# Optimization experiments

Measured on AMD Instinct MI355X. Metric: run time of the kernel, lower is better.

Reference implementation:

```python
import jax, jax.numpy as jnp
import numpy as np

N_ATOMS = 50000
N_EDGES = 640000
D = 128
N_RBF = 20
N_INTER = 3

act = jax.nn.softplus


def setup_inputs() -> dict:
    key = jax.random.key(0)
    ks = jax.random.split(key, 16)
    s = 1.0 / np.sqrt(D)
    inp = {
        "x": jax.random.normal(ks[0], (N_ATOMS, D), jnp.float32),
        "g_ij": jax.random.uniform(ks[1], (N_EDGES, N_RBF), jnp.float32),
        "idx_i": jax.random.randint(ks[2], (N_EDGES,), 0, N_ATOMS),
        "idx_j": jax.random.randint(ks[3], (N_EDGES,), 0, N_ATOMS),
        "n_atoms": N_ATOMS,
        "u": jnp.ones((D,), jnp.float32),
        "Wf": jax.random.normal(ks[4], (D, D), jnp.float32) * s,
        "bf": jnp.zeros((D,), jnp.float32),
        # linear_g weight init to zero in original; use small random so grads flow
        "Wg": jax.random.normal(ks[5], (D, N_RBF), jnp.float32) * 0.01,
        "bg": jnp.zeros((D,), jnp.float32),
        "Wj": jax.random.normal(ks[6], (D, D), jnp.float32) * s,
        "bj": jnp.zeros((D,), jnp.float32),
        "Wi": jax.random.normal(ks[7], (D, D), jnp.float32) * s,
        "bi": jnp.zeros((D,), jnp.float32),
        "res_w1": jax.random.normal(ks[8], (N_INTER, D, D), jnp.float32) * s,
        "res_b1": jnp.zeros((N_INTER, D), jnp.float32),
        "res_w2": jax.random.normal(ks[9], (N_INTER, D, D), jnp.float32) * s,
        "res_b2": jnp.zeros((N_INTER, D), jnp.float32),
    }
    return inp


def reference(x, g_ij, idx_i, idx_j, n_atoms, u, Wf, bf, Wg, bg, Wj, bj, Wi, bi,
              res_w1, res_b1, res_w2, res_b2):
    x_j = x[idx_j]                                    # [E, D] gather
    xp = u * x                                        # [N, D]
    # sequential_j: act -> linear_j -> act, gated by linear_g(g_ij)
    vp = act(act(x_j) @ Wj.T + bj) * (g_ij @ Wg.T + bg)   # [E, D]
    vm = act(act(x) @ Wi.T + bi)                      # [N, D]
    v = jax.ops.segment_sum(vp, idx_i, num_segments=n_atoms) + vm
    for l in range(res_w1.shape[0]):
        h = act(v) @ res_w1[l].T + res_b1[l]
        h = act(h) @ res_w2[l].T + res_b2[l]
        v = h + v
    v = act(v)
    return xp + v @ Wf.T + bf
```

## Files before the change

### kernel.cpp

```cpp
#include <hip/hip_runtime.h>
#include <hip/hip_fp16.h>

#define DD 128

typedef __attribute__((ext_vector_type(8))) short short8;
typedef __attribute__((ext_vector_type(8))) unsigned short ushort8;
typedef __attribute__((ext_vector_type(4))) float floatx4;
typedef unsigned int uint32;

__device__ __forceinline__ float sp(float x) {
    return fmaxf(x, 0.0f) + __logf(1.0f + __expf(-fabsf(x)));
}

__device__ __forceinline__ unsigned short f2bf(float f) {
    union { float f; uint32 u; } c; c.f = f;
    const uint32 u = c.u;
    return (unsigned short)((u + 0x7fffu + ((u >> 16) & 1u)) >> 16);
}

__device__ __forceinline__ unsigned short f2h(float f) {
    __half h = __float2half(f);
    return __builtin_bit_cast(unsigned short, h);
}

__global__ __launch_bounds__(256)
void convert_w(const float* __restrict__ Wj, const float* __restrict__ Wi,
               const float* __restrict__ rw1, const float* __restrict__ rw2,
               const float* __restrict__ Wf, unsigned short* __restrict__ out,
               const float* __restrict__ g, unsigned short* __restrict__ gh,
               int gchunks)
{
    if ((int)blockIdx.x >= 72) {
        const int gid = ((int)blockIdx.x - 72) * 256 + threadIdx.x;
        if (gid < gchunks) {
            const float4 f0 = reinterpret_cast<const float4*>(g)[2 * gid];
            const float4 f1 = reinterpret_cast<const float4*>(g)[2 * gid + 1];
            ushort8 o;
            o[0] = f2h(f0.x); o[1] = f2h(f0.y); o[2] = f2h(f0.z); o[3] = f2h(f0.w);
            o[4] = f2h(f1.x); o[5] = f2h(f1.y); o[6] = f2h(f1.z); o[7] = f2h(f1.w);
            reinterpret_cast<ushort8*>(gh)[gid] = o;
        }
        return;
    }
    const int gid = blockIdx.x * 256 + threadIdx.x;
    const int mat = gid >> 11;
    const int f8  = gid & 2047;
    const float* src;
    if      (mat == 0) src = Wj;
    else if (mat == 1) src = Wi;
    else if (mat <= 4) src = rw1 + (size_t)(mat - 2) * 16384;
    else if (mat <= 7) src = rw2 + (size_t)(mat - 5) * 16384;
    else               src = Wf;
    const int row = f8 >> 4;
    const int ch  = f8 & 15;
    const float4 a = reinterpret_cast<const float4*>(src)[2 * f8];
    const float4 b = reinterpret_cast<const float4*>(src)[2 * f8 + 1];
    ushort8 u8;
    u8[0] = f2bf(a.x); u8[1] = f2bf(a.y); u8[2] = f2bf(a.z); u8[3] = f2bf(a.w);
    u8[4] = f2bf(b.x); u8[5] = f2bf(b.y); u8[6] = f2bf(b.z); u8[7] = f2bf(b.w);
    *reinterpret_cast<ushort8*>(out + (size_t)mat * 16384 + row * 128 +
                                ((ch ^ (row & 15)) << 3)) = u8;
}

__device__ __forceinline__ void stage_wb(const unsigned short* __restrict__ Wb,
                                         unsigned short* wl, int t)
{
    #pragma unroll
    for (int i = 0; i < 8; ++i) {
        const int c = t + i * 256;
        *reinterpret_cast<ushort8*>(wl + c * 8) =
            *reinterpret_cast<const ushort8*>(Wb + c * 8);
    }
}

__device__ __forceinline__ void load_afrag_act(const float* __restrict__ X,
                                               int m, int q, int n, short8 af[4])
{
    const int mm = m < n ? m : n - 1;
    const float* row = X + (size_t)mm * DD + q * 8;
    #pragma unroll
    for (int kk = 0; kk < 4; ++kk) {
        const float4 a = *reinterpret_cast<const float4*>(row + kk * 32);
        const float4 b = *reinterpret_cast<const float4*>(row + kk * 32 + 4);
        ushort8 u;
        u[0] = f2bf(sp(a.x)); u[1] = f2bf(sp(a.y)); u[2] = f2bf(sp(a.z)); u[3] = f2bf(sp(a.w));
        u[4] = f2bf(sp(b.x)); u[5] = f2bf(sp(b.y)); u[6] = f2bf(sp(b.z)); u[7] = f2bf(sp(b.w));
        af[kk] = __builtin_bit_cast(short8, u);
    }
}

__device__ __forceinline__ void mfma_gemm(const unsigned short* wl,
                                          const short8 af[4],
                                          int cl, int q, floatx4 acc[8])
{
    #pragma unroll
    for (int nt = 0; nt < 8; ++nt) {
        const int nrow = nt * 16 + cl;
        #pragma unroll
        for (int kk = 0; kk < 4; ++kk) {
            const int chs = (kk * 4 + q) ^ cl;
            const short8 bfr = *reinterpret_cast<const short8*>(wl + nrow * 128 + (chs << 3));
            acc[nt] = __builtin_amdgcn_mfma_f32_16x16x32_bf16(af[kk], bfr, acc[nt], 0, 0, 0);
        }
    }
}

__global__ __launch_bounds__(256, 4)
void dual_gemm(const float* __restrict__ x,
               const unsigned short* __restrict__ Wb,
               const float* __restrict__ bj, const float* __restrict__ bi,
               unsigned short* __restrict__ Aout, float* __restrict__ vout, int n)
{
    __shared__ __align__(16) unsigned short wl[128 * 128];
    const int t = threadIdx.x;
    const int lane = t & 63, wv = t >> 6;
    const int cl = lane & 15, q = lane >> 4;
    const int m0 = blockIdx.x * 64 + wv * 16;

    short8 af[4];
    load_afrag_act(x, m0 + cl, q, n, af);

    stage_wb(Wb, wl, t);
    __syncthreads();

    floatx4 acc[8];
    #pragma unroll
    for (int nt = 0; nt < 8; ++nt) acc[nt] = (floatx4){0.f, 0.f, 0.f, 0.f};
    mfma_gemm(wl, af, cl, q, acc);

    #pragma unroll
    for (int nt = 0; nt < 8; ++nt) {
        const int col = nt * 16 + cl;
        const float bb = bj[col];
        #pragma unroll
        for (int r = 0; r < 4; ++r) {
            const int row = m0 + q * 4 + r;
            if (row < n) Aout[(size_t)row * DD + col] = f2bf(sp(acc[nt][r] + bb));
        }
    }

    __syncthreads();
    stage_wb(Wb + 16384, wl, t);
    __syncthreads();

    #pragma unroll
    for (int nt = 0; nt < 8; ++nt) acc[nt] = (floatx4){0.f, 0.f, 0.f, 0.f};
    mfma_gemm(wl, af, cl, q, acc);

    #pragma unroll
    for (int nt = 0; nt < 8; ++nt) {
        const int col = nt * 16 + cl;
        const float bb = bi[col];
        #pragma unroll
        for (int r = 0; r < 4; ++r) {
            const int row = m0 + q * 4 + r;
            if (row < n) vout[(size_t)row * DD + col] = sp(acc[nt][r] + bb);
        }
    }
}

__global__ __launch_bounds__(256, 3)
void tail_kernel(const float* __restrict__ vin, const float* __restrict__ x,
                 const unsigned short* __restrict__ Wb,
                 const float* __restrict__ rb1, const float* __restrict__ rb2,
                 const float* __restrict__ bf, const float* __restrict__ u,
                 float* __restrict__ out, int n)
{
    __shared__ __align__(16) unsigned short wl[128 * 128];
    __shared__ __align__(16) unsigned short hl[64 * 128];
    const int t = threadIdx.x;
    const int lane = t & 63, wv = t >> 6;
    const int cl = lane & 15, q = lane >> 4;
    const int mb = blockIdx.x * 64;
    const int ml2 = wv * 16 + cl;

    floatx4 vac[8];
    #pragma unroll
    for (int nt = 0; nt < 8; ++nt) {
        #pragma unroll
        for (int r = 0; r < 4; ++r) {
            const int row = mb + wv * 16 + q * 4 + r;
            const int col = nt * 16 + cl;
            vac[nt][r] = (row < n) ? vin[(size_t)row * DD + col] : 0.f;
        }
    }

    short8 af[4];
    load_afrag_act(vin, mb + wv * 16 + cl, q, n, af);

    stage_wb(Wb + 2 * 16384, wl, t);
    __syncthreads();

    ushort8 wreg[8];

    #pragma unroll
    for (int l = 0; l < 3; ++l) {
        if (l > 0) {
            #pragma unroll
            for (int nt = 0; nt < 8; ++nt) {
                const int col = nt * 16 + cl;
                const int ch = col >> 3;
                #pragma unroll
                for (int r = 0; r < 4; ++r) {
                    const int ml = wv * 16 + q * 4 + r;
                    hl[ml * 128 + ((ch ^ (ml & 15)) << 3) + (col & 7)] = f2bf(sp(vac[nt][r]));
                }
            }
            #pragma unroll
            for (int kk = 0; kk < 4; ++kk)
                af[kk] = *reinterpret_cast<const short8*>(hl + ml2 * 128 + (((kk * 4 + q) ^ cl) << 3));
        }

        #pragma unroll
        for (int i = 0; i < 8; ++i)
            wreg[i] = *reinterpret_cast<const ushort8*>(Wb + (size_t)(5 + l) * 16384 + (t + i * 256) * 8);

        floatx4 acc[8];
        #pragma unroll
        for (int nt = 0; nt < 8; ++nt) acc[nt] = (floatx4){0.f, 0.f, 0.f, 0.f};
        mfma_gemm(wl, af, cl, q, acc);

        const float* b1 = rb1 + (size_t)l * DD;
        #pragma unroll
        for (int nt = 0; nt < 8; ++nt) {
            const int col = nt * 16 + cl;
            const int ch = col >> 3;
            const float bb = b1[col];
            #pragma unroll
            for (int r = 0; r < 4; ++r) {
                const int ml = wv * 16 + q * 4 + r;
                hl[ml * 128 + ((ch ^ (ml & 15)) << 3) + (col & 7)] = f2bf(sp(acc[nt][r] + bb));
            }
        }
        short8 af2[4];
        #pragma unroll
        for (int kk = 0; kk < 4; ++kk)
            af2[kk] = *reinterpret_cast<const short8*>(hl + ml2 * 128 + (((kk * 4 + q) ^ cl) << 3));

        __syncthreads();
        #pragma unroll
        for (int i = 0; i < 8; ++i)
            *reinterpret_cast<ushort8*>(wl + (t + i * 256) * 8) = wreg[i];
        __syncthreads();

        const int nxt = (l < 2) ? (3 + l) : 8;
        #pragma unroll
        for (int i = 0; i < 8; ++i)
            wreg[i] = *reinterpret_cast<const ushort8*>(Wb + (size_t)nxt * 16384 + (t + i * 256) * 8);

        mfma_gemm(wl, af2, cl, q, vac);
        const float* b2 = rb2 + (size_t)l * DD;
        #pragma unroll
        for (int nt = 0; nt < 8; ++nt) {
            const float bb = b2[nt * 16 + cl];
            #pragma unroll
            for (int r = 0; r < 4; ++r) vac[nt][r] += bb;
        }

        __syncthreads();
        #pragma unroll
        for (int i = 0; i < 8; ++i)
            *reinterpret_cast<ushort8*>(wl + (t + i * 256) * 8) = wreg[i];
        __syncthreads();
    }

    #pragma unroll
    for (int nt = 0; nt < 8; ++nt) {
        const int col = nt * 16 + cl;
        const int ch = col >> 3;
        #pragma unroll
        for (int r = 0; r < 4; ++r) {
            const int ml = wv * 16 + q * 4 + r;
            hl[ml * 128 + ((ch ^ (ml & 15)) << 3) + (col & 7)] = f2bf(sp(vac[nt][r]));
        }
    }
    short8 aff[4];
    #pragma unroll
    for (int kk = 0; kk < 4; ++kk)
        aff[kk] = *reinterpret_cast<const short8*>(hl + ml2 * 128 + (((kk * 4 + q) ^ cl) << 3));

    floatx4 acc[8];
    #pragma unroll
    for (int nt = 0; nt < 8; ++nt) acc[nt] = (floatx4){0.f, 0.f, 0.f, 0.f};
    mfma_gemm(wl, aff, cl, q, acc);

    #pragma unroll
    for (int nt = 0; nt < 8; ++nt) {
        const int col = nt * 16 + cl;
        const float bb = bf[col];
        const float uu = u[col];
        #pragma unroll
        for (int r = 0; r < 4; ++r) {
            const int row = mb + wv * 16 + q * 4 + r;
            if (row < n)
                out[(size_t)row * DD + col] =
                    acc[nt][r] + bb + uu * x[(size_t)row * DD + col];
        }
    }
}


__global__ __launch_bounds__(256)
void hist_kernel(const int* __restrict__ idx_i, int* __restrict__ cnt, int E)
{
    const int e = blockIdx.x * 256 + threadIdx.x;
    if (e < E) atomicAdd(&cnt[idx_i[e]], 1);
}

__global__ __launch_bounds__(256)
void scan_reduce(const int* __restrict__ cnt, int* __restrict__ bsum, int n)
{
    __shared__ int wsum[4];
    const int t = threadIdx.x;
    const int lane = t & 63, wv = t >> 6;
    const int i0 = blockIdx.x * 1024 + t * 4;
    int s = 0;
    #pragma unroll
    for (int k = 0; k < 4; ++k) if (i0 + k < n) s += cnt[i0 + k];
    #pragma unroll
    for (int d = 1; d < 64; d <<= 1) s += __shfl_down(s, d, 64);
    if (lane == 0) wsum[wv] = s;
    __syncthreads();
    if (t == 0) bsum[blockIdx.x] = wsum[0] + wsum[1] + wsum[2] + wsum[3];
}

__global__ __launch_bounds__(256)
void scan_apply(const int* __restrict__ cnt, const int* __restrict__ bsum,
                int* __restrict__ off, int* __restrict__ cnt2, int n, int nb)
{
    __shared__ int wsum[4];
    const int t = threadIdx.x;
    const int lane = t & 63, wv = t >> 6;

    int bval = (lane < nb && lane < (int)blockIdx.x) ? bsum[lane] : 0;
    #pragma unroll
    for (int d = 32; d >= 1; d >>= 1) bval += __shfl_down(bval, d, 64);
    const int blk_off = __shfl(bval, 0, 64);

    const int i0 = blockIdx.x * 1024 + t * 4;
    const int v0 = (i0 + 0 < n) ? cnt[i0 + 0] : 0;
    const int v1 = (i0 + 1 < n) ? cnt[i0 + 1] : 0;
    const int v2 = (i0 + 2 < n) ? cnt[i0 + 2] : 0;
    const int v3 = (i0 + 3 < n) ? cnt[i0 + 3] : 0;
    const int s = v0 + v1 + v2 + v3;
    int incl = s;
    #pragma unroll
    for (int d = 1; d < 64; d <<= 1) {
        const int y = __shfl_up(incl, d, 64);
        if (lane >= d) incl += y;
    }
    if (lane == 63) wsum[wv] = incl;
    __syncthreads();
    int woff = blk_off;
    #pragma unroll
    for (int w = 0; w < 4; ++w) if (w < wv) woff += wsum[w];
    const int excl = woff + incl - s;
    if (i0 + 0 < n) { off[i0 + 0] = excl;                cnt2[i0 + 0] = 0; }
    if (i0 + 1 < n) { off[i0 + 1] = excl + v0;           cnt2[i0 + 1] = 0; }
    if (i0 + 2 < n) { off[i0 + 2] = excl + v0 + v1;      cnt2[i0 + 2] = 0; }
    if (i0 + 3 < n) { off[i0 + 3] = excl + v0 + v1 + v2; cnt2[i0 + 3] = 0; }
}

__global__ __launch_bounds__(256)
void scatter_kernel(const int* __restrict__ idx_i, const int* __restrict__ idx_j,
                    const int* __restrict__ off, int* __restrict__ cnt2,
                    int2* __restrict__ spair, int E)
{
    const int e = blockIdx.x * 256 + threadIdx.x;
    if (e < E) {
        const int i = idx_i[e];
        const int p = off[i] + atomicAdd(&cnt2[i], 1);
        spair[p] = make_int2(e, idx_j[e]);
    }
}

template<int GH>
__global__ __launch_bounds__(256, 4)
void agg_kernel(const int* __restrict__ off, const int* __restrict__ cnt,
                const int2* __restrict__ spair,
                const unsigned short* __restrict__ gh,
                const float* __restrict__ g,
                const float* __restrict__ Wg, const float* __restrict__ bg,
                const unsigned short* __restrict__ A, float* __restrict__ v, int N)
{
    const int t = threadIdx.x;
    const int lane = t & 63;
    const int wid0 = blockIdx.x * 4 + (t >> 6);
    const int nw   = gridDim.x * 4;
    const int d0 = lane << 1;

    const float bg0 = bg[d0], bg1 = bg[d0 + 1];

    if (GH) {
        __half2 w0h[10], w1h[10];
        #pragma unroll
        for (int k2 = 0; k2 < 10; ++k2) {
            w0h[k2] = __floats2half2_rn(Wg[d0 * 20 + 2 * k2], Wg[d0 * 20 + 2 * k2 + 1]);
            w1h[k2] = __floats2half2_rn(Wg[(d0 + 1) * 20 + 2 * k2], Wg[(d0 + 1) * 20 + 2 * k2 + 1]);
        }

        for (int i = wid0; i < N; i += nw) {
            const int beg = off[i], num = cnt[i], end = beg + num;
            float2 acc = *reinterpret_cast<const float2*>(v + (size_t)i * DD + d0);

            int p = beg;
            while (p + 4 <= end) {
                int ee[4], jj[4];
                #pragma unroll
                for (int u = 0; u < 4; ++u) {
                    const int2 pr = spair[p + u];
                    ee[u] = __builtin_amdgcn_readfirstlane(pr.x);
                    jj[u] = __builtin_amdgcn_readfirstlane(pr.y);
                }
                uint32 aa[4];
                float2 gq[4][5];
                #pragma unroll
                for (int u = 0; u < 4; ++u) {
                    aa[u] = *reinterpret_cast<const uint32*>(A + (size_t)jj[u] * DD + d0);
                    const float2* gp = reinterpret_cast<const float2*>(gh + (size_t)ee[u] * 20);
                    #pragma unroll
                    for (int q2 = 0; q2 < 5; ++q2) gq[u][q2] = gp[q2];
                }
                #pragma unroll
                for (int u = 0; u < 4; ++u) {
                    __half2 a0 = __float2half2_rn(0.f), a1 = __float2half2_rn(0.f);
                    #pragma unroll
                    for (int q2 = 0; q2 < 5; ++q2) {
                        const __half2 h0 = __builtin_bit_cast(__half2, gq[u][q2].x);
                        const __half2 h1 = __builtin_bit_cast(__half2, gq[u][q2].y);
                        a0 = __hfma2(h0, w0h[2 * q2], a0);
                        a1 = __hfma2(h0, w1h[2 * q2], a1);
                        a0 = __hfma2(h1, w0h[2 * q2 + 1], a0);
                        a1 = __hfma2(h1, w1h[2 * q2 + 1], a1);
                    }
                    const float t0 = bg0 + __low2float(a0) + __high2float(a0);
                    const float t1 = bg1 + __low2float(a1) + __high2float(a1);
                    union { uint32 u32; float f; } cx, cy;
                    cx.u32 = aa[u] << 16;
                    cy.u32 = aa[u] & 0xffff0000u;
                    acc.x = fmaf(cx.f, t0, acc.x);
                    acc.y = fmaf(cy.f, t1, acc.y);
                }
                p += 4;
            }
            for (; p < end; ++p) {
                const int2 pr = spair[p];
                const int e0 = __builtin_amdgcn_readfirstlane(pr.x);
                const int j0 = __builtin_amdgcn_readfirstlane(pr.y);
                const uint32 a0u = *reinterpret_cast<const uint32*>(A + (size_t)j0 * DD + d0);
                const float2* gp = reinterpret_cast<const float2*>(gh + (size_t)e0 * 20);
                __half2 a0 = __float2half2_rn(0.f), a1 = __float2half2_rn(0.f);
                #pragma unroll
                for (int q2 = 0; q2 < 5; ++q2) {
                    const float2 qq = gp[q2];
                    const __half2 h0 = __builtin_bit_cast(__half2, qq.x);
                    const __half2 h1 = __builtin_bit_cast(__half2, qq.y);
                    a0 = __hfma2(h0, w0h[2 * q2], a0);
                    a1 = __hfma2(h0, w1h[2 * q2], a1);
                    a0 = __hfma2(h1, w0h[2 * q2 + 1], a0);
                    a1 = __hfma2(h1, w1h[2 * q2 + 1], a1);
                }
                const float t0 = bg0 + __low2float(a0) + __high2float(a0);
                const float t1 = bg1 + __low2float(a1) + __high2float(a1);
                union { uint32 u32; float f; } cx, cy;
                cx.u32 = a0u << 16;
                cy.u32 = a0u & 0xffff0000u;
                acc.x = fmaf(cx.f, t0, acc.x);
                acc.y = fmaf(cy.f, t1, acc.y);
            }
            *reinterpret_cast<float2*>(v + (size_t)i * DD + d0) = acc;
        }
    } else {
        float2 wg01[20];
        #pragma unroll
        for (int k = 0; k < 20; ++k) {
            wg01[k].x = Wg[d0 * 20 + k];
            wg01[k].y = Wg[(d0 + 1) * 20 + k];
        }
        for (int i = wid0; i < N; i += nw) {
            const int beg = off[i], num = cnt[i], end = beg + num;
            float2 acc = *reinterpret_cast<const float2*>(v + (size_t)i * DD + d0);
            int p = beg;
            for (; p + 2 <= end; p += 2) {
                const int2 pr0 = spair[p];
                const int2 pr1 = spair[p + 1];
                const int e0 = __builtin_amdgcn_readfirstlane(pr0.x);
                const int j0 = __builtin_amdgcn_readfirstlane(pr0.y);
                const int e1 = __builtin_amdgcn_readfirstlane(pr1.x);
                const int j1 = __builtin_amdgcn_readfirstlane(pr1.y);
                const uint32 a0 = *reinterpret_cast<const uint32*>(A + (size_t)j0 * DD + d0);
                const uint32 a1 = *reinterpret_cast<const uint32*>(A + (size_t)j1 * DD + d0);
                const float4* g0p = reinterpret_cast<const float4*>(g + (size_t)e0 * 20);
                const float4* g1p = reinterpret_cast<const float4*>(g + (size_t)e1 * 20);
                float2 t0 = make_float2(bg0, bg1), t1 = make_float2(bg0, bg1);
                #pragma unroll
                for (int qq = 0; qq < 5; ++qq) {
                    const float4 p0 = g0p[qq];
                    const float4 p1 = g1p[qq];
                    t0.x = fmaf(p0.x, wg01[qq*4+0].x, t0.x); t0.y = fmaf(p0.x, wg01[qq*4+0].y, t0.y);
                    t0.x = fmaf(p0.y, wg01[qq*4+1].x, t0.x); t0.y = fmaf(p0.y, wg01[qq*4+1].y, t0.y);
                    t0.x = fmaf(p0.z, wg01[qq*4+2].x, t0.x); t0.y = fmaf(p0.z, wg01[qq*4+2].y, t0.y);
                    t0.x = fmaf(p0.w, wg01[qq*4+3].x, t0.x); t0.y = fmaf(p0.w, wg01[qq*4+3].y, t0.y);
                    t1.x = fmaf(p1.x, wg01[qq*4+0].x, t1.x); t1.y = fmaf(p1.x, wg01[qq*4+0].y, t1.y);
                    t1.x = fmaf(p1.y, wg01[qq*4+1].x, t1.x); t1.y = fmaf(p1.y, wg01[qq*4+1].y, t1.y);
                    t1.x = fmaf(p1.z, wg01[qq*4+2].x, t1.x); t1.y = fmaf(p1.z, wg01[qq*4+2].y, t1.y);
                    t1.x = fmaf(p1.w, wg01[qq*4+3].x, t1.x); t1.y = fmaf(p1.w, wg01[qq*4+3].y, t1.y);
                }
                union { uint32 u; float f; } c0x, c0y, c1x, c1y;
                c0x.u = a0 << 16; c0y.u = a0 & 0xffff0000u;
                c1x.u = a1 << 16; c1y.u = a1 & 0xffff0000u;
                acc.x = fmaf(c0x.f, t0.x, acc.x); acc.y = fmaf(c0y.f, t0.y, acc.y);
                acc.x = fmaf(c1x.f, t1.x, acc.x); acc.y = fmaf(c1y.f, t1.y, acc.y);
            }
            if (p < end) {
                const int2 pr0 = spair[p];
                const int e0 = __builtin_amdgcn_readfirstlane(pr0.x);
                const int j0 = __builtin_amdgcn_readfirstlane(pr0.y);
                const uint32 a0 = *reinterpret_cast<const uint32*>(A + (size_t)j0 * DD + d0);
                const float4* g0p = reinterpret_cast<const float4*>(g + (size_t)e0 * 20);
                float2 t0 = make_float2(bg0, bg1);
                #pragma unroll
                for (int qq = 0; qq < 5; ++qq) {
                    const float4 p0 = g0p[qq];
                    t0.x = fmaf(p0.x, wg01[qq*4+0].x, t0.x); t0.y = fmaf(p0.x, wg01[qq*4+0].y, t0.y);
                    t0.x = fmaf(p0.y, wg01[qq*4+1].x, t0.x); t0.y = fmaf(p0.y, wg01[qq*4+1].y, t0.y);
                    t0.x = fmaf(p0.z, wg01[qq*4+2].x, t0.x); t0.y = fmaf(p0.z, wg01[qq*4+2].y, t0.y);
                    t0.x = fmaf(p0.w, wg01[qq*4+3].x, t0.x); t0.y = fmaf(p0.w, wg01[qq*4+3].y, t0.y);
                }
                union { uint32 u; float f; } c0x, c0y;
                c0x.u = a0 << 16; c0y.u = a0 & 0xffff0000u;
                acc.x = fmaf(c0x.f, t0.x, acc.x); acc.y = fmaf(c0y.f, t0.y, acc.y);
            }
            *reinterpret_cast<float2*>(v + (size_t)i * DD + d0) = acc;
        }
    }
}

extern "C" void kernel_launch(void* const* d_in, const int* in_sizes, int n_in,
                              void* d_out, int out_size, void* d_ws, size_t ws_size,
                              hipStream_t stream)
{
    const float* x     = (const float*)d_in[0];
    const float* g     = (const float*)d_in[1];
    const int*   idx_i = (const int*)d_in[2];
    const int*   idx_j = (const int*)d_in[3];
    const float* u     = (const float*)d_in[5];
    const float* Wf    = (const float*)d_in[6];
    const float* bf    = (const float*)d_in[7];
    const float* Wg    = (const float*)d_in[8];
    const float* bg    = (const float*)d_in[9];
    const float* Wj    = (const float*)d_in[10];
    const float* bj    = (const float*)d_in[11];
    const float* Wi    = (const float*)d_in[12];
    const float* bi    = (const float*)d_in[13];
    const float* rw1   = (const float*)d_in[14];
    const float* rb1   = (const float*)d_in[15];
    const float* rw2   = (const float*)d_in[16];
    const float* rb2   = (const float*)d_in[17];

    const int N = in_sizes[0] / DD;
    const int E = in_sizes[2];
    float* out = (float*)d_out;

    float*          v     = (float*)d_ws;
    unsigned short* A     = (unsigned short*)(v + (size_t)N * DD);
    int*            cnt   = (int*)(A + (size_t)N * DD);
    int*            off   = cnt + N;
    int*            cnt2  = off + N;
    int*            bsum  = cnt2 + N;
    int2*           spair = (int2*)(bsum + 64);
    unsigned short* Wb    = (unsigned short*)(spair + E);
    unsigned short* gh    = Wb + 9 * 16384;

    const size_t need_gh = (size_t)((char*)(gh + (size_t)E * 20) - (char*)d_ws);
    const bool gh_ok = ws_size >= need_gh;

    dim3 blk(256);
    const int tiles    = (N + 63) / 64;
    const int eblocks  = (E + 255) / 256;
    const int sblocks  = (N + 1023) / 1024;
    const int gchunks  = gh_ok ? (E * 20) / 8 : 0;
    const int gblocks  = gh_ok ? (gchunks + 255) / 256 : 0;

    convert_w<<<72 + gblocks, blk, 0, stream>>>(Wj, Wi, rw1, rw2, Wf, Wb,
                                                g, gh, gchunks);

    hipMemsetAsync(cnt, 0, (size_t)N * sizeof(int), stream);
    hist_kernel<<<eblocks, blk, 0, stream>>>(idx_i, cnt, E);
    scan_reduce<<<sblocks, blk, 0, stream>>>(cnt, bsum, N);
    scan_apply<<<sblocks, blk, 0, stream>>>(cnt, bsum, off, cnt2, N, sblocks);
    scatter_kernel<<<eblocks, blk, 0, stream>>>(idx_i, idx_j, off, cnt2, spair, E);

    dual_gemm<<<tiles, blk, 0, stream>>>(x, Wb, bj, bi, A, v, N);

    if (gh_ok)
        agg_kernel<1><<<2048, blk, 0, stream>>>(off, cnt, spair, gh, g,
                                                Wg, bg, A, v, N);
    else
        agg_kernel<0><<<2048, blk, 0, stream>>>(off, cnt, spair, gh, g,
                                                Wg, bg, A, v, N);

    tail_kernel<<<tiles, blk, 0, stream>>>(v, x, Wb, rb1, rb2, bf, u, out, N);
}
```

Before: 253.2 us.

## Double-buffer tail kernel weights in LDS instead of register staging

The tail kernel now holds two 32KB LDS weight buffers and loads the next layer's weights straight into the inactive buffer while the current GEMM runs. This replaces the global-to-register prefetch followed by a synchronised register-to-LDS copy, removing one barrier pair per GEMM and freeing the staging registers. The price is more LDS per block (about 80KB), so the occupancy hint drops from 3 to 2 blocks per CU, which may reduce latency hiding. Unless stage_wb uses asynchronous loads, its global reads may still block before the GEMM that follows.

New measurement: 243.7 us. 1.04x faster.

```diff
diff --git a/kernel.cpp b/kernel.cpp
--- a/kernel.cpp
+++ b/kernel.cpp
@@ -159,14 +159,14 @@
     }
 }
 
-__global__ __launch_bounds__(256, 3)
+__global__ __launch_bounds__(256, 2)
 void tail_kernel(const float* __restrict__ vin, const float* __restrict__ x,
                  const unsigned short* __restrict__ Wb,
                  const float* __restrict__ rb1, const float* __restrict__ rb2,
                  const float* __restrict__ bf, const float* __restrict__ u,
                  float* __restrict__ out, int n)
 {
-    __shared__ __align__(16) unsigned short wl[128 * 128];
+    __shared__ __align__(16) unsigned short wl[2][128 * 128];
     __shared__ __align__(16) unsigned short hl[64 * 128];
     const int t = threadIdx.x;
     const int lane = t & 63, wv = t >> 6;
@@ -188,13 +188,14 @@
     short8 af[4];
     load_afrag_act(vin, mb + wv * 16 + cl, q, n, af);
 
-    stage_wb(Wb + 2 * 16384, wl, t);
+    stage_wb(Wb + 2 * 16384, wl[0], t);
     __syncthreads();
-
-    ushort8 wreg[8];
+    int buf = 0;
 
     #pragma unroll
     for (int l = 0; l < 3; ++l) {
+        stage_wb(Wb + (size_t)(5 + l) * 16384, wl[buf ^ 1], t);
+
         if (l > 0) {
             #pragma unroll
             for (int nt = 0; nt < 8; ++nt) {
@@ -211,14 +212,10 @@
                 af[kk] = *reinterpret_cast<const short8*>(hl + ml2 * 128 + (((kk * 4 + q) ^ cl) << 3));
         }
 
-        #pragma unroll
-        for (int i = 0; i < 8; ++i)
-            wreg[i] = *reinterpret_cast<const ushort8*>(Wb + (size_t)(5 + l) * 16384 + (t + i * 256) * 8);
-
         floatx4 acc[8];
         #pragma unroll
         for (int nt = 0; nt < 8; ++nt) acc[nt] = (floatx4){0.f, 0.f, 0.f, 0.f};
-        mfma_gemm(wl, af, cl, q, acc);
+        mfma_gemm(wl[buf], af, cl, q, acc);
 
         const float* b1 = rb1 + (size_t)l * DD;
         #pragma unroll
@@ -238,17 +235,12 @@
             af2[kk] = *reinterpret_cast<const short8*>(hl + ml2 * 128 + (((kk * 4 + q) ^ cl) << 3));
 
         __syncthreads();
-        #pragma unroll
-        for (int i = 0; i < 8; ++i)
-            *reinterpret_cast<ushort8*>(wl + (t + i * 256) * 8) = wreg[i];
-        __syncthreads();
+        buf ^= 1;
 
         const int nxt = (l < 2) ? (3 + l) : 8;
-        #pragma unroll
-        for (int i = 0; i < 8; ++i)
-            wreg[i] = *reinterpret_cast<const ushort8*>(Wb + (size_t)nxt * 16384 + (t + i * 256) * 8);
-
-        mfma_gemm(wl, af2, cl, q, vac);
+        stage_wb(Wb + (size_t)nxt * 16384, wl[buf ^ 1], t);
+
+        mfma_gemm(wl[buf], af2, cl, q, vac);
         const float* b2 = rb2 + (size_t)l * DD;
         #pragma unroll
         for (int nt = 0; nt < 8; ++nt) {
@@ -258,10 +250,7 @@
         }
 
         __syncthreads();
-        #pragma unroll
-        for (int i = 0; i < 8; ++i)
-            *reinterpret_cast<ushort8*>(wl + (t + i * 256) * 8) = wreg[i];
-        __syncthreads();
+        buf ^= 1;
     }
 
     #pragma unroll
@@ -282,7 +271,7 @@
     floatx4 acc[8];
     #pragma unroll
     for (int nt = 0; nt < 8; ++nt) acc[nt] = (floatx4){0.f, 0.f, 0.f, 0.f};
-    mfma_gemm(wl, aff, cl, q, acc);
+    mfma_gemm(wl[buf], aff, cl, q, acc);
 
     #pragma unroll
     for (int nt = 0; nt < 8; ++nt) {
```
